# Optimization experiments

Hardware: AMD Instinct MI355X
Metric: run time of the kernel (lower is better)

Reference implementation:

```python
import jax, jax.numpy as jnp
import numpy as np

EMBED_DIM = 512
NUM_HEADS = 8
HEAD_DIM = EMBED_DIM // NUM_HEADS
BATCH = 2
SEQ = 4096
LN_EPS = 1e-5


def setup_inputs() -> dict:
    key = jax.random.key(0)
    ks = jax.random.split(key, 10)
    s = 1.0 / np.sqrt(EMBED_DIM)
    d = dict(
        x=jax.random.normal(ks[0], (BATCH, SEQ, EMBED_DIM), dtype=jnp.float32),
        wq=jax.random.normal(ks[1], (EMBED_DIM, EMBED_DIM), dtype=jnp.float32) * s,
        bq=jnp.zeros((EMBED_DIM,), jnp.float32),
        wk=jax.random.normal(ks[2], (EMBED_DIM, EMBED_DIM), dtype=jnp.float32) * s,
        bk=jnp.zeros((EMBED_DIM,), jnp.float32),
        wv=jax.random.normal(ks[3], (EMBED_DIM, EMBED_DIM), dtype=jnp.float32) * s,
        bv=jnp.zeros((EMBED_DIM,), jnp.float32),
        wo=jax.random.normal(ks[4], (EMBED_DIM, EMBED_DIM), dtype=jnp.float32) * s,
        bo=jnp.zeros((EMBED_DIM,), jnp.float32),
        ln_g=jnp.ones((EMBED_DIM,), jnp.float32),
        ln_b=jnp.zeros((EMBED_DIM,), jnp.float32),
    )
    return d


def reference(x, wq, bq, wk, bk, wv, bv, wo, bo, ln_g, ln_b):
    B, S, E = x.shape
    H, D = NUM_HEADS, HEAD_DIM
    residual = x
    # QKV projections (weights stored [in, out])
    q = (x @ wq + bq).reshape(B, S, H, D).transpose(0, 2, 1, 3)  # [B,H,S,D]
    k = (x @ wk + bk).reshape(B, S, H, D).transpose(0, 2, 1, 3)
    v = (x @ wv + bv).reshape(B, S, H, D).transpose(0, 2, 1, 3)
    # scaled dot-product attention
    scores = jnp.einsum('bhsd,bhtd->bhst', q, k) / jnp.sqrt(jnp.float32(D))
    attn = jax.nn.softmax(scores, axis=-1)
    ctx = jnp.einsum('bhst,bhtd->bhsd', attn, v)  # [B,H,S,D]
    ctx = ctx.transpose(0, 2, 1, 3).reshape(B, S, E)
    # output projection (dropout=0 in eval) + residual + LayerNorm
    out = ctx @ wo + bo
    y = out + residual
    mu = jnp.mean(y, axis=-1, keepdims=True)
    var = jnp.var(y, axis=-1, keepdims=True)
    y = (y - mu) * jax.lax.rsqrt(var + LN_EPS) * ln_g + ln_b
    return y
```

## Files before the change

kernel.cpp:

```cpp
#include <hip/hip_runtime.h>


typedef unsigned short u16;
typedef unsigned int u32;
typedef short bf16x8 __attribute__((ext_vector_type(8)));
typedef float f32x2 __attribute__((ext_vector_type(2)));
typedef float f32x4 __attribute__((ext_vector_type(4)));
typedef float f32x8 __attribute__((ext_vector_type(8)));
typedef float f32x16 __attribute__((ext_vector_type(16)));
typedef unsigned short u16x4 __attribute__((ext_vector_type(4)));
typedef unsigned int u32x2 __attribute__((ext_vector_type(2)));
typedef unsigned int u32x4 __attribute__((ext_vector_type(4)));

#define S_LEN 4096
#define E_DIM 512
#define H_NUM 8
#define D_DIM 64
#define M_ROWS 8192

#define Q_SCALE 0.18033688011112042f

static __device__ __forceinline__ u16 f2bf(float f) {
    unsigned int u = __float_as_uint(f);
    u += 0x7fffu + ((u >> 16) & 1u);
    return (u16)(u >> 16);
}

static __device__ __forceinline__ u32 cvt_pk_bf16(float a, float b) {
    u32 r;
    asm("v_cvt_pk_bf16_f32 %0, %1, %2" : "=v"(r) : "v"(a), "v"(b));
    return r;
}

#if __has_builtin(__builtin_amdgcn_exp2f)
#define EXP2(x) __builtin_amdgcn_exp2f(x)
#else
static __device__ __forceinline__ float exp2_hw(float x) {
    float r;
    asm volatile("v_exp_f32 %0, %1\n\ts_nop 1" : "=v"(r) : "v"(x));
    return r;
}
#define EXP2(x) exp2_hw(x)
#endif

static __device__ __forceinline__ float vsum16(f32x16 v) {
    f32x8 a = __builtin_shufflevector(v, v, 0, 1, 2, 3, 4, 5, 6, 7) +
              __builtin_shufflevector(v, v, 8, 9, 10, 11, 12, 13, 14, 15);
    f32x4 b = __builtin_shufflevector(a, a, 0, 1, 2, 3) +
              __builtin_shufflevector(a, a, 4, 5, 6, 7);
    f32x2 c = __builtin_shufflevector(b, b, 0, 1) +
              __builtin_shufflevector(b, b, 2, 3);
    return c[0] + c[1];
}

static __device__ __forceinline__ void gload_lds16(const u16* g, u16* l) {
    __builtin_amdgcn_global_load_lds(
        (const __attribute__((address_space(1))) u32*)g,
        (__attribute__((address_space(3))) u32*)l, 16, 0, 0);
}

__global__ __launch_bounds__(256) void cvt_k(const float* __restrict__ src,
                                             u16* __restrict__ dst, int n4) {
    int i = blockIdx.x * 256 + threadIdx.x;
    if (i >= n4) return;
    float4 v = ((const float4*)src)[i];
    u16x4 o;
    o[0] = f2bf(v.x); o[1] = f2bf(v.y); o[2] = f2bf(v.z); o[3] = f2bf(v.w);
    ((u16x4*)dst)[i] = o;
}

__global__ __launch_bounds__(256) void cvtT4_k(
    const float* __restrict__ w0, const float* __restrict__ w1,
    const float* __restrict__ w2, const float* __restrict__ w3,
    u16* __restrict__ o0, u16* __restrict__ o1,
    u16* __restrict__ o2, u16* __restrict__ o3)
{
    __shared__ float fT[64][68];
    const int g = blockIdx.x;
    const int which = g >> 6;
    const int tile = g & 63;
    const int k0 = (tile >> 3) * 64, n0 = (tile & 7) * 64;
    const float* w = which == 0 ? w0 : which == 1 ? w1 : which == 2 ? w2 : w3;
    u16* o = which == 0 ? o0 : which == 1 ? o1 : which == 2 ? o2 : o3;
    const int tr = threadIdx.x >> 4, tc = threadIdx.x & 15;
    #pragma unroll
    for (int p = 0; p < 4; p++) {
        const int kr = p * 16 + tr;
        float4 v = *(const float4*)&w[(size_t)(k0 + kr) * 512 + n0 + tc * 4];
        fT[tc * 4 + 0][kr] = v.x;
        fT[tc * 4 + 1][kr] = v.y;
        fT[tc * 4 + 2][kr] = v.z;
        fT[tc * 4 + 3][kr] = v.w;
    }
    __syncthreads();
    #pragma unroll
    for (int p = 0; p < 4; p++) {
        const int nr = p * 16 + tr;
        u16x4 ov;
        ov[0] = f2bf(fT[nr][tc * 4 + 0]);
        ov[1] = f2bf(fT[nr][tc * 4 + 1]);
        ov[2] = f2bf(fT[nr][tc * 4 + 2]);
        ov[3] = f2bf(fT[nr][tc * 4 + 3]);
        *(u16x4*)&o[(size_t)(n0 + nr) * 512 + k0 + tc * 4] = ov;
    }
}

template <int BM, int BN, int MODE>
__global__ __launch_bounds__(256) void gemm_k(
    const u16* __restrict__ A,
    const u16* __restrict__ Wt0, const u16* __restrict__ Wt1,
    const u16* __restrict__ Wt2,
    const float* __restrict__ b0, const float* __restrict__ b1,
    const float* __restrict__ b2,
    u16* __restrict__ q_out, u16* __restrict__ k_out, u16* __restrict__ vt_out,
    const float* __restrict__ resid, float* __restrict__ of32)
{
    constexpr int FM = BM / 32, FN = BN / 32;
    __shared__ __align__(16) u16 Asm[BM * 32];
    __shared__ __align__(16) u16 Bsm[BN * 32];

    const int t = threadIdx.x, wave = t >> 6, lane = t & 63;
    constexpr int nb_per = 512 / BN;
    int sel, bn;
    if (MODE == 0) { sel = blockIdx.x / nb_per; bn = blockIdx.x % nb_per; }
    else           { sel = 0;                   bn = blockIdx.x; }
    const int bm = blockIdx.y;

    const u16* Wt = (MODE == 0) ? (sel == 0 ? Wt0 : (sel == 1 ? Wt1 : Wt2)) : Wt0;
    const float* bias = (MODE == 0) ? (sel == 0 ? b0 : (sel == 1 ? b1 : b2)) : b0;

    const int wm = (wave >> 1) * (BM / 2);
    const int wn = (wave & 1) * (BN / 2);
    const int lrow = lane & 15, kq = (lane >> 4) * 8;

    f32x4 acc[FM][FN];
    #pragma unroll
    for (int i = 0; i < FM; i++)
        #pragma unroll
        for (int j = 0; j < FN; j++)
            acc[i][j] = (f32x4){0.f, 0.f, 0.f, 0.f};

    const u16* Ag = A + (size_t)bm * BM * 512 + (size_t)(t >> 2) * 512 + (t & 3) * 8;
    const u16* Bg = Wt + (size_t)bn * BN * 512 + (size_t)(t >> 2) * 512 + (t & 3) * 8;
    u16* Al = Asm + (size_t)wave * 512;
    u16* Bl = Bsm + (size_t)wave * 512;

    for (int kk = 0; kk < 512; kk += 32) {
        #pragma unroll
        for (int p = 0; p < BM / 32; p++)
            gload_lds16(Ag + (size_t)p * 64 * 512 + kk, Al + p * 2048);
        #pragma unroll
        for (int p = 0; p < BN / 32; p++)
            gload_lds16(Bg + (size_t)p * 64 * 512 + kk, Bl + p * 2048);
        __syncthreads();

        bf16x8 af[FM], bfv[FN];
        #pragma unroll
        for (int i = 0; i < FM; i++)
            af[i] = *(const bf16x8*)&Asm[(wm + i * 16 + lrow) * 32 + kq];
        #pragma unroll
        for (int j = 0; j < FN; j++)
            bfv[j] = *(const bf16x8*)&Bsm[(wn + j * 16 + lrow) * 32 + kq];
        #pragma unroll
        for (int i = 0; i < FM; i++)
            #pragma unroll
            for (int j = 0; j < FN; j++)
                acc[i][j] = __builtin_amdgcn_mfma_f32_16x16x32_bf16(
                    af[i], bfv[j], acc[i][j], 0, 0, 0);
        __syncthreads();
    }

    #pragma unroll
    for (int i = 0; i < FM; i++) {
        #pragma unroll
        for (int j = 0; j < FN; j++) {
            const int col = bn * BN + wn + j * 16 + lrow;
            const float bcol = bias[col];
            const int row0 = bm * BM + wm + i * 16 + (lane >> 4) * 4;
            if (MODE == 0) {
                const int b = row0 >> 12, s0v = row0 & 4095;
                const int h = col >> 6,  d = col & 63;
                if (sel == 2) {
                    u16x4 pk;
                    #pragma unroll
                    for (int q = 0; q < 4; q++)
                        pk[q] = f2bf(acc[i][j][q] + bcol);
                    *(u16x4*)&vt_out[(((size_t)(b * 8 + h)) * 64 + d) * 4096 + s0v] = pk;
                } else {
                    u16* o = (sel == 0) ? q_out : k_out;
                    const float sc = (sel == 0) ? Q_SCALE : 1.0f;
                    #pragma unroll
                    for (int q = 0; q < 4; q++)
                        o[(((size_t)(b * 8 + h)) * 4096 + s0v + q) * 64 + d] =
                            f2bf((acc[i][j][q] + bcol) * sc);
                }
            } else {
                #pragma unroll
                for (int q = 0; q < 4; q++) {
                    const size_t idx = (size_t)(row0 + q) * 512 + col;
                    of32[idx] = acc[i][j][q] + bcol + resid[idx];
                }
            }
        }
    }
}

__global__ __launch_bounds__(512, 2) void attn_k(
    const u16* __restrict__ Q, const u16* __restrict__ K,
    const u16* __restrict__ Vt, u16* __restrict__ ctx)
{
    __shared__ __align__(16) u16 SM[32768];

    const int t = threadIdx.x, w = t >> 6, lane = t & 63;
    const int l31 = lane & 31, hi = lane >> 5;
    const int kh = w >> 2, wl = w & 3;

    const int bid = blockIdx.x;
    const int xcd = bid & 7, j = bid >> 3;
    const int head = xcd * 2 + (j & 1);
    const int qt = j >> 1;

    const u16* Qb = Q + (size_t)head * S_LEN * D_DIM;
    const u16* Kb = K + (size_t)head * S_LEN * D_DIM;
    const u16* Vb = Vt + (size_t)head * D_DIM * S_LEN;
    const int q0w = qt * 256 + wl * 64;

    bf16x8 qfA[4], qfB[4];
    #pragma unroll
    for (int ks = 0; ks < 4; ks++) {
        qfA[ks] = *(const bf16x8*)&Qb[(size_t)(q0w + l31) * 64 + ks * 16 + hi * 8];
        qfB[ks] = *(const bf16x8*)&Qb[(size_t)(q0w + 32 + l31) * 64 + ks * 16 + hi * 8];
    }

    u16* const KH = SM + kh * 16384;
    u16* const VH = KH + 8192;

    const u16* kp[8];
    const u16* vp[8];
    #pragma unroll
    for (int i = 0; i < 8; i++) {
        const int r = (i >> 2) * 32 + l31;
        const int c = (i & 3) * 2 + hi;
        const int phys = r * 8 + (c ^ (r & 7));
        kp[i] = KH + phys * 8;
        vp[i] = VH + phys * 8;
    }

    f32x16 acc0A = {0.f}, acc1A = {0.f}, acc0B = {0.f}, acc1B = {0.f};
    float lA = 0.f, lB = 0.f;

    const int th = t & 255;
    const int c0 = th, c1 = th + 256;
    const int sr0 = c0 >> 3, sc0 = (c0 & 7) ^ (sr0 & 7);
    const int sr1 = c1 >> 3, sc1 = (c1 & 7) ^ (sr1 & 7);
    const u16* kg0 = Kb + (size_t)(kh * 2048 + sr0) * 64 + sc0 * 8;
    const u16* kg1 = Kb + (size_t)(kh * 2048 + sr1) * 64 + sc1 * 8;
    const u16* vg0 = Vb + (size_t)sr0 * S_LEN + kh * 2048 + sc0 * 8;
    const u16* vg1 = Vb + (size_t)sr1 * S_LEN + kh * 2048 + sc1 * 8;
    u16* const kd0 = KH + wl * 512;
    u16* const kd1 = KH + 2048 + wl * 512;
    u16* const vd0 = VH + wl * 512;
    u16* const vd1 = VH + 2048 + wl * 512;

#define ATTN_STAGE(DST)                                                      \
    {                                                                        \
        gload_lds16(kg0, kd0 + (DST)); gload_lds16(kg1, kd1 + (DST));        \
        gload_lds16(vg0, vd0 + (DST)); gload_lds16(vg1, vd1 + (DST));        \
        kg0 += 4096; kg1 += 4096; vg0 += 64; vg1 += 64;                      \
    }

#define ATTN_COMPUTE(BUF)                                                    \
    {                                                                        \
        f32x16 sA0 = {0.f}, sA1 = {0.f}, sB0 = {0.f}, sB1 = {0.f};           \
        __builtin_amdgcn_s_setprio(1);                                       \
        _Pragma("unroll")                                                    \
        for (int ks = 0; ks < 4; ks++) {                                     \
            bf16x8 ka = *(const bf16x8*)(kp[ks] + (BUF));                    \
            bf16x8 kb2 = *(const bf16x8*)(kp[4 + ks] + (BUF));               \
            sA0 = __builtin_amdgcn_mfma_f32_32x32x16_bf16(ka, qfA[ks], sA0, 0, 0, 0); \
            sB0 = __builtin_amdgcn_mfma_f32_32x32x16_bf16(ka, qfB[ks], sB0, 0, 0, 0); \
            sA1 = __builtin_amdgcn_mfma_f32_32x32x16_bf16(kb2, qfA[ks], sA1, 0, 0, 0); \
            sB1 = __builtin_amdgcn_mfma_f32_32x32x16_bf16(kb2, qfB[ks], sB1, 0, 0, 0); \
        }                                                                    \
        __builtin_amdgcn_s_setprio(0);                                       \
        _Pragma("unroll")                                                    \
        for (int e = 0; e < 16; e++) {                                       \
            sA0[e] = EXP2(sA0[e]); sA1[e] = EXP2(sA1[e]);                    \
            sB0[e] = EXP2(sB0[e]); sB1[e] = EXP2(sB1[e]);                    \
        }                                                                    \
        lA += vsum16(sA0 + sA1);                                             \
        lB += vsum16(sB0 + sB1);                                             \
        bf16x8 pfA[4], pfB[4];                                               \
        _Pragma("unroll")                                                    \
        for (int ks = 0; ks < 4; ks++) {                                     \
            const int r0 = (ks & 1) * 8;                                     \
            const f32x16& sa = (ks < 2) ? sA0 : sA1;                         \
            u32 ax1 = cvt_pk_bf16(sa[r0 + 0], sa[r0 + 1]);                   \
            u32 ay1 = cvt_pk_bf16(sa[r0 + 4], sa[r0 + 5]);                   \
            asm("v_permlane32_swap_b32 %0, %1" : "+v"(ax1), "+v"(ay1));      \
            u32 ax2 = cvt_pk_bf16(sa[r0 + 2], sa[r0 + 3]);                   \
            u32 ay2 = cvt_pk_bf16(sa[r0 + 6], sa[r0 + 7]);                   \
            asm("v_permlane32_swap_b32 %0, %1" : "+v"(ax2), "+v"(ay2));      \
            u32x4 wva; wva[0] = ax1; wva[1] = ax2; wva[2] = ay1; wva[3] = ay2; \
            pfA[ks] = *(bf16x8*)&wva;                                        \
            const f32x16& sb = (ks < 2) ? sB0 : sB1;                         \
            u32 bx1 = cvt_pk_bf16(sb[r0 + 0], sb[r0 + 1]);                   \
            u32 by1 = cvt_pk_bf16(sb[r0 + 4], sb[r0 + 5]);                   \
            asm("v_permlane32_swap_b32 %0, %1" : "+v"(bx1), "+v"(by1));      \
            u32 bx2 = cvt_pk_bf16(sb[r0 + 2], sb[r0 + 3]);                   \
            u32 by2 = cvt_pk_bf16(sb[r0 + 6], sb[r0 + 7]);                   \
            asm("v_permlane32_swap_b32 %0, %1" : "+v"(bx2), "+v"(by2));      \
            u32x4 wvb; wvb[0] = bx1; wvb[1] = bx2; wvb[2] = by1; wvb[3] = by2; \
            pfB[ks] = *(bf16x8*)&wvb;                                        \
        }                                                                    \
        __builtin_amdgcn_s_setprio(1);                                       \
        _Pragma("unroll")                                                    \
        for (int ks = 0; ks < 4; ks++) {                                     \
            bf16x8 va = *(const bf16x8*)(vp[ks] + (BUF));                    \
            bf16x8 vb2 = *(const bf16x8*)(vp[4 + ks] + (BUF));               \
            acc0A = __builtin_amdgcn_mfma_f32_32x32x16_bf16(va, pfA[ks], acc0A, 0, 0, 0); \
            acc0B = __builtin_amdgcn_mfma_f32_32x32x16_bf16(va, pfB[ks], acc0B, 0, 0, 0); \
            acc1A = __builtin_amdgcn_mfma_f32_32x32x16_bf16(vb2, pfA[ks], acc1A, 0, 0, 0); \
            acc1B = __builtin_amdgcn_mfma_f32_32x32x16_bf16(vb2, pfB[ks], acc1B, 0, 0, 0); \
        }                                                                    \
        __builtin_amdgcn_s_setprio(0);                                       \
    }

    ATTN_STAGE(0);
    __syncthreads();

    for (int it = 0; it < 16; ++it) {
        ATTN_STAGE(4096);
        ATTN_COMPUTE(0);
        __syncthreads();
        if (it != 15) ATTN_STAGE(0);
        ATTN_COMPUTE(4096);
        __syncthreads();
    }

    __syncthreads();
    float* const cb = (float*)SM;
    float* const p = cb + (size_t)(wl * 64 + lane) * 34;
    if (kh == 1) {
        #pragma unroll
        for (int e = 0; e < 16; e++) { p[e] = acc0A[e]; p[16 + e] = acc0B[e]; }
        p[32] = lA; p[33] = lB;
    }
    __syncthreads();
    if (kh == 0) {
        #pragma unroll
        for (int e = 0; e < 16; e++) { acc0A[e] += p[e]; acc0B[e] += p[16 + e]; }
        lA += p[32]; lB += p[33];
    }
    __syncthreads();
    if (kh == 1) {
        #pragma unroll
        for (int e = 0; e < 16; e++) { p[e] = acc1A[e]; p[16 + e] = acc1B[e]; }
    }
    __syncthreads();
    if (kh == 0) {
        #pragma unroll
        for (int e = 0; e < 16; e++) { acc1A[e] += p[e]; acc1B[e] += p[16 + e]; }
        lA += __shfl_xor(lA, 32);
        lB += __shfl_xor(lB, 32);

        const int b = head >> 3, h = head & 7;
        const float liA = 1.0f / lA, liB = 1.0f / lB;
        const size_t oA = (size_t)(b * S_LEN + q0w + l31) * 512 + h * 64 + 4 * hi;
        const size_t oB = oA + (size_t)32 * 512;
        #pragma unroll
        for (int rq = 0; rq < 4; rq++) {
            u32x2 wa;
            wa[0] = cvt_pk_bf16(acc0A[4 * rq + 0] * liA, acc0A[4 * rq + 1] * liA);
            wa[1] = cvt_pk_bf16(acc0A[4 * rq + 2] * liA, acc0A[4 * rq + 3] * liA);
            *(u32x2*)&ctx[oA + 8 * rq] = wa;
            wa[0] = cvt_pk_bf16(acc1A[4 * rq + 0] * liA, acc1A[4 * rq + 1] * liA);
            wa[1] = cvt_pk_bf16(acc1A[4 * rq + 2] * liA, acc1A[4 * rq + 3] * liA);
            *(u32x2*)&ctx[oA + 32 + 8 * rq] = wa;
            wa[0] = cvt_pk_bf16(acc0B[4 * rq + 0] * liB, acc0B[4 * rq + 1] * liB);
            wa[1] = cvt_pk_bf16(acc0B[4 * rq + 2] * liB, acc0B[4 * rq + 3] * liB);
            *(u32x2*)&ctx[oB + 8 * rq] = wa;
            wa[0] = cvt_pk_bf16(acc1B[4 * rq + 0] * liB, acc1B[4 * rq + 1] * liB);
            wa[1] = cvt_pk_bf16(acc1B[4 * rq + 2] * liB, acc1B[4 * rq + 3] * liB);
            *(u32x2*)&ctx[oB + 32 + 8 * rq] = wa;
        }
    }
#undef ATTN_STAGE
#undef ATTN_COMPUTE
}

__global__ __launch_bounds__(256) void ln_k(const float* __restrict__ y,
                                            const float* __restrict__ g,
                                            const float* __restrict__ beta,
                                            float* __restrict__ out)
{
    const int w = threadIdx.x >> 6, lane = threadIdx.x & 63;
    const size_t row = (size_t)blockIdx.x * 4 + w;
    const float4* yr = (const float4*)(y + row * 512);
    float4 a = yr[lane], b = yr[lane + 64];
    float s  = a.x + a.y + a.z + a.w + b.x + b.y + b.z + b.w;
    float ss = a.x*a.x + a.y*a.y + a.z*a.z + a.w*a.w
             + b.x*b.x + b.y*b.y + b.z*b.z + b.w*b.w;
    #pragma unroll
    for (int o = 1; o < 64; o <<= 1) {
        s  += __shfl_xor(s, o);
        ss += __shfl_xor(ss, o);
    }
    const float mu  = s * (1.0f / 512.0f);
    const float var = ss * (1.0f / 512.0f) - mu * mu;
    const float inv = rsqrtf(var + 1e-5f);
    const float4* g4 = (const float4*)g;
    const float4* b4 = (const float4*)beta;
    float4 ga = g4[lane], gb = g4[lane + 64];
    float4 ba = b4[lane], bb = b4[lane + 64];
    float4 oa, ob;
    oa.x = (a.x - mu) * inv * ga.x + ba.x;
    oa.y = (a.y - mu) * inv * ga.y + ba.y;
    oa.z = (a.z - mu) * inv * ga.z + ba.z;
    oa.w = (a.w - mu) * inv * ga.w + ba.w;
    ob.x = (b.x - mu) * inv * gb.x + bb.x;
    ob.y = (b.y - mu) * inv * gb.y + bb.y;
    ob.z = (b.z - mu) * inv * gb.z + bb.z;
    ob.w = (b.w - mu) * inv * gb.w + bb.w;
    float4* orow = (float4*)(out + row * 512);
    orow[lane] = oa;
    orow[lane + 64] = ob;
}

extern "C" void kernel_launch(void* const* d_in, const int* in_sizes, int n_in,
                              void* d_out, int out_size, void* d_ws, size_t ws_size,
                              hipStream_t stream)
{
    const float* x    = (const float*)d_in[0];
    const float* wq   = (const float*)d_in[1];
    const float* bq   = (const float*)d_in[2];
    const float* wk   = (const float*)d_in[3];
    const float* bk   = (const float*)d_in[4];
    const float* wv   = (const float*)d_in[5];
    const float* bv   = (const float*)d_in[6];
    const float* wo   = (const float*)d_in[7];
    const float* bo   = (const float*)d_in[8];
    const float* ln_g = (const float*)d_in[9];
    const float* ln_b = (const float*)d_in[10];

    char* ws = (char*)d_ws;
    u16* xb   = (u16*)(ws);
    u16* wqt  = (u16*)(ws + 8388608);
    u16* wkt  = (u16*)(ws + 8912896);
    u16* wvt  = (u16*)(ws + 9437184);
    u16* wot  = (u16*)(ws + 9961472);
    u16* Qb   = (u16*)(ws + 10485760);
    u16* Kb   = (u16*)(ws + 18874368);
    u16* Vtb  = (u16*)(ws + 27262976);
    u16* ctxb = (u16*)(ws + 35651584);
    float* yb = (float*)(ws + 10485760);

    cvt_k<<<4096, 256, 0, stream>>>(x, xb, (M_ROWS * E_DIM) / 4);
    cvtT4_k<<<256, 256, 0, stream>>>(wq, wk, wv, wo, wqt, wkt, wvt, wot);

    gemm_k<128, 128, 0><<<dim3(12, 64), 256, 0, stream>>>(
        xb, wqt, wkt, wvt, bq, bk, bv, Qb, Kb, Vtb, nullptr, nullptr);

    attn_k<<<256, 512, 0, stream>>>(Qb, Kb, Vtb, ctxb);

    gemm_k<128, 64, 2><<<dim3(8, 64), 256, 0, stream>>>(
        ctxb, wot, wot, wot, bo, bo, bo, nullptr, nullptr, nullptr, x, yb);

    ln_k<<<2048, 256, 0, stream>>>(yb, ln_g, ln_b, (float*)d_out);
}
```

Measured before the change: 150.9 us.

## Split attention KV range across four wave groups with 1024-thread blocks

The attention kernel now launches 1024 threads per block, giving four groups of four waves. Each group processes a quarter of the key/value sequence, using 32-key tiles per stage instead of 64, and the LDS layout and swizzle are reworked to match. Partial outputs and row sums are then reduced through shared memory in four combine rounds. The aim is more waves per block to hide latency, at the cost of smaller MFMA batches per stage, more barriers in the reduction, and a lower per-thread register budget.

```diff
diff --git a/kernel.cpp b/kernel.cpp
--- a/kernel.cpp
+++ b/kernel.cpp
@@ -205,7 +205,7 @@
     }
 }
 
-__global__ __launch_bounds__(512, 2) void attn_k(
+__global__ __launch_bounds__(1024) void attn_k(
     const u16* __restrict__ Q, const u16* __restrict__ K,
     const u16* __restrict__ Vt, u16* __restrict__ ctx)
 {
@@ -232,96 +232,87 @@
         qfB[ks] = *(const bf16x8*)&Qb[(size_t)(q0w + 32 + l31) * 64 + ks * 16 + hi * 8];
     }
 
-    u16* const KH = SM + kh * 16384;
-    u16* const VH = KH + 8192;
-
-    const u16* kp[8];
-    const u16* vp[8];
-    #pragma unroll
-    for (int i = 0; i < 8; i++) {
-        const int r = (i >> 2) * 32 + l31;
-        const int c = (i & 3) * 2 + hi;
-        const int phys = r * 8 + (c ^ (r & 7));
-        kp[i] = KH + phys * 8;
-        vp[i] = VH + phys * 8;
+    u16* const KQ = SM + kh * 8192;
+
+    const u16* kp[4];
+    const u16* vp[4];
+    #pragma unroll
+    for (int ks = 0; ks < 4; ks++) {
+        const int c = ks * 2 + hi;
+        kp[ks] = KQ + (l31 * 8 + (c ^ (l31 & 7))) * 8;
+    }
+    #pragma unroll
+    for (int i = 0; i < 4; i++) {
+        const int dblk = i >> 1, ks2 = i & 1;
+        const int r = dblk * 32 + l31;
+        const int c = ks2 * 2 + hi;
+        vp[i] = KQ + 4096 + (r * 4 + (c ^ ((r >> 1) & 3))) * 8;
     }
 
     f32x16 acc0A = {0.f}, acc1A = {0.f}, acc0B = {0.f}, acc1B = {0.f};
     float lA = 0.f, lB = 0.f;
 
     const int th = t & 255;
-    const int c0 = th, c1 = th + 256;
-    const int sr0 = c0 >> 3, sc0 = (c0 & 7) ^ (sr0 & 7);
-    const int sr1 = c1 >> 3, sc1 = (c1 & 7) ^ (sr1 & 7);
-    const u16* kg0 = Kb + (size_t)(kh * 2048 + sr0) * 64 + sc0 * 8;
-    const u16* kg1 = Kb + (size_t)(kh * 2048 + sr1) * 64 + sc1 * 8;
-    const u16* vg0 = Vb + (size_t)sr0 * S_LEN + kh * 2048 + sc0 * 8;
-    const u16* vg1 = Vb + (size_t)sr1 * S_LEN + kh * 2048 + sc1 * 8;
-    u16* const kd0 = KH + wl * 512;
-    u16* const kd1 = KH + 2048 + wl * 512;
-    u16* const vd0 = VH + wl * 512;
-    u16* const vd1 = VH + 2048 + wl * 512;
+    const int kr = th >> 3, kc = (th & 7) ^ (kr & 7);
+    const int vr = th >> 2, vc = (th & 3) ^ ((vr >> 1) & 3);
+    const u16* kg = Kb + (size_t)(kh * 1024 + kr) * 64 + kc * 8;
+    const u16* vg = Vb + (size_t)vr * S_LEN + kh * 1024 + vc * 8;
+    u16* const kd = KQ + wl * 512;
+    u16* const vd = KQ + 4096 + wl * 512;
 
 #define ATTN_STAGE(DST)                                                      \
     {                                                                        \
-        gload_lds16(kg0, kd0 + (DST)); gload_lds16(kg1, kd1 + (DST));        \
-        gload_lds16(vg0, vd0 + (DST)); gload_lds16(vg1, vd1 + (DST));        \
-        kg0 += 4096; kg1 += 4096; vg0 += 64; vg1 += 64;                      \
+        gload_lds16(kg, kd + (DST)); gload_lds16(vg, vd + (DST));            \
+        kg += 2048; vg += 32;                                                \
     }
 
 #define ATTN_COMPUTE(BUF)                                                    \
     {                                                                        \
-        f32x16 sA0 = {0.f}, sA1 = {0.f}, sB0 = {0.f}, sB1 = {0.f};           \
+        f32x16 sA = {0.f}, sB = {0.f};                                       \
         __builtin_amdgcn_s_setprio(1);                                       \
         _Pragma("unroll")                                                    \
         for (int ks = 0; ks < 4; ks++) {                                     \
             bf16x8 ka = *(const bf16x8*)(kp[ks] + (BUF));                    \
-            bf16x8 kb2 = *(const bf16x8*)(kp[4 + ks] + (BUF));               \
-            sA0 = __builtin_amdgcn_mfma_f32_32x32x16_bf16(ka, qfA[ks], sA0, 0, 0, 0); \
-            sB0 = __builtin_amdgcn_mfma_f32_32x32x16_bf16(ka, qfB[ks], sB0, 0, 0, 0); \
-            sA1 = __builtin_amdgcn_mfma_f32_32x32x16_bf16(kb2, qfA[ks], sA1, 0, 0, 0); \
-            sB1 = __builtin_amdgcn_mfma_f32_32x32x16_bf16(kb2, qfB[ks], sB1, 0, 0, 0); \
+            sA = __builtin_amdgcn_mfma_f32_32x32x16_bf16(ka, qfA[ks], sA, 0, 0, 0); \
+            sB = __builtin_amdgcn_mfma_f32_32x32x16_bf16(ka, qfB[ks], sB, 0, 0, 0); \
         }                                                                    \
         __builtin_amdgcn_s_setprio(0);                                       \
         _Pragma("unroll")                                                    \
         for (int e = 0; e < 16; e++) {                                       \
-            sA0[e] = EXP2(sA0[e]); sA1[e] = EXP2(sA1[e]);                    \
-            sB0[e] = EXP2(sB0[e]); sB1[e] = EXP2(sB1[e]);                    \
+            sA[e] = EXP2(sA[e]); sB[e] = EXP2(sB[e]);                        \
         }                                                                    \
-        lA += vsum16(sA0 + sA1);                                             \
-        lB += vsum16(sB0 + sB1);                                             \
-        bf16x8 pfA[4], pfB[4];                                               \
-        _Pragma("unroll")                                                    \
-        for (int ks = 0; ks < 4; ks++) {                                     \
-            const int r0 = (ks & 1) * 8;                                     \
-            const f32x16& sa = (ks < 2) ? sA0 : sA1;                         \
-            u32 ax1 = cvt_pk_bf16(sa[r0 + 0], sa[r0 + 1]);                   \
-            u32 ay1 = cvt_pk_bf16(sa[r0 + 4], sa[r0 + 5]);                   \
+        lA += vsum16(sA);                                                    \
+        lB += vsum16(sB);                                                    \
+        bf16x8 pfA[2], pfB[2];                                               \
+        _Pragma("unroll")                                                    \
+        for (int ks2 = 0; ks2 < 2; ks2++) {                                  \
+            const int r0 = ks2 * 8;                                          \
+            u32 ax1 = cvt_pk_bf16(sA[r0 + 0], sA[r0 + 1]);                   \
+            u32 ay1 = cvt_pk_bf16(sA[r0 + 4], sA[r0 + 5]);                   \
             asm("v_permlane32_swap_b32 %0, %1" : "+v"(ax1), "+v"(ay1));      \
-            u32 ax2 = cvt_pk_bf16(sa[r0 + 2], sa[r0 + 3]);                   \
-            u32 ay2 = cvt_pk_bf16(sa[r0 + 6], sa[r0 + 7]);                   \
+            u32 ax2 = cvt_pk_bf16(sA[r0 + 2], sA[r0 + 3]);                   \
+            u32 ay2 = cvt_pk_bf16(sA[r0 + 6], sA[r0 + 7]);                   \
             asm("v_permlane32_swap_b32 %0, %1" : "+v"(ax2), "+v"(ay2));      \
             u32x4 wva; wva[0] = ax1; wva[1] = ax2; wva[2] = ay1; wva[3] = ay2; \
-            pfA[ks] = *(bf16x8*)&wva;                                        \
-            const f32x16& sb = (ks < 2) ? sB0 : sB1;                         \
-            u32 bx1 = cvt_pk_bf16(sb[r0 + 0], sb[r0 + 1]);                   \
-            u32 by1 = cvt_pk_bf16(sb[r0 + 4], sb[r0 + 5]);                   \
+            pfA[ks2] = *(bf16x8*)&wva;                                       \
+            u32 bx1 = cvt_pk_bf16(sB[r0 + 0], sB[r0 + 1]);                   \
+            u32 by1 = cvt_pk_bf16(sB[r0 + 4], sB[r0 + 5]);                   \
             asm("v_permlane32_swap_b32 %0, %1" : "+v"(bx1), "+v"(by1));      \
-            u32 bx2 = cvt_pk_bf16(sb[r0 + 2], sb[r0 + 3]);                   \
-            u32 by2 = cvt_pk_bf16(sb[r0 + 6], sb[r0 + 7]);                   \
+            u32 bx2 = cvt_pk_bf16(sB[r0 + 2], sB[r0 + 3]);                   \
+            u32 by2 = cvt_pk_bf16(sB[r0 + 6], sB[r0 + 7]);                   \
             asm("v_permlane32_swap_b32 %0, %1" : "+v"(bx2), "+v"(by2));      \
             u32x4 wvb; wvb[0] = bx1; wvb[1] = bx2; wvb[2] = by1; wvb[3] = by2; \
-            pfB[ks] = *(bf16x8*)&wvb;                                        \
+            pfB[ks2] = *(bf16x8*)&wvb;                                       \
         }                                                                    \
         __builtin_amdgcn_s_setprio(1);                                       \
         _Pragma("unroll")                                                    \
-        for (int ks = 0; ks < 4; ks++) {                                     \
-            bf16x8 va = *(const bf16x8*)(vp[ks] + (BUF));                    \
-            bf16x8 vb2 = *(const bf16x8*)(vp[4 + ks] + (BUF));               \
-            acc0A = __builtin_amdgcn_mfma_f32_32x32x16_bf16(va, pfA[ks], acc0A, 0, 0, 0); \
-            acc0B = __builtin_amdgcn_mfma_f32_32x32x16_bf16(va, pfB[ks], acc0B, 0, 0, 0); \
-            acc1A = __builtin_amdgcn_mfma_f32_32x32x16_bf16(vb2, pfA[ks], acc1A, 0, 0, 0); \
-            acc1B = __builtin_amdgcn_mfma_f32_32x32x16_bf16(vb2, pfB[ks], acc1B, 0, 0, 0); \
+        for (int ks2 = 0; ks2 < 2; ks2++) {                                  \
+            bf16x8 v0 = *(const bf16x8*)(vp[ks2] + (BUF));                   \
+            bf16x8 v1 = *(const bf16x8*)(vp[2 + ks2] + (BUF));               \
+            acc0A = __builtin_amdgcn_mfma_f32_32x32x16_bf16(v0, pfA[ks2], acc0A, 0, 0, 0); \
+            acc0B = __builtin_amdgcn_mfma_f32_32x32x16_bf16(v0, pfB[ks2], acc0B, 0, 0, 0); \
+            acc1A = __builtin_amdgcn_mfma_f32_32x32x16_bf16(v1, pfA[ks2], acc1A, 0, 0, 0); \
+            acc1B = __builtin_amdgcn_mfma_f32_32x32x16_bf16(v1, pfB[ks2], acc1B, 0, 0, 0); \
         }                                                                    \
         __builtin_amdgcn_s_setprio(0);                                       \
     }
@@ -330,37 +321,40 @@
     __syncthreads();
 
     for (int it = 0; it < 16; ++it) {
-        ATTN_STAGE(4096);
+        ATTN_STAGE(2048);
         ATTN_COMPUTE(0);
         __syncthreads();
         if (it != 15) ATTN_STAGE(0);
-        ATTN_COMPUTE(4096);
+        ATTN_COMPUTE(2048);
         __syncthreads();
     }
 
-    __syncthreads();
     float* const cb = (float*)SM;
-    float* const p = cb + (size_t)(wl * 64 + lane) * 34;
-    if (kh == 1) {
-        #pragma unroll
-        for (int e = 0; e < 16; e++) { p[e] = acc0A[e]; p[16 + e] = acc0B[e]; }
-        p[32] = lA; p[33] = lB;
-    }
-    __syncthreads();
+#define COMBINE(ACC, EXTRA_W, EXTRA_R)                                       \
+    __syncthreads();                                                         \
+    if (kh) {                                                                \
+        float* p = cb + (size_t)(((kh - 1) * 4 + wl) * 64 + lane) * 17;      \
+        _Pragma("unroll")                                                    \
+        for (int e = 0; e < 16; e++) p[e] = ACC[e];                          \
+        EXTRA_W;                                                             \
+    }                                                                        \
+    __syncthreads();                                                         \
+    if (!kh) {                                                               \
+        _Pragma("unroll")                                                    \
+        for (int jj = 0; jj < 3; jj++) {                                     \
+            const float* p = cb + (size_t)((jj * 4 + wl) * 64 + lane) * 17;  \
+            _Pragma("unroll")                                                \
+            for (int e = 0; e < 16; e++) ACC[e] += p[e];                     \
+            EXTRA_R;                                                         \
+        }                                                                    \
+    }
+    COMBINE(acc0A, p[16] = lA, lA += p[16])
+    COMBINE(acc0B, p[16] = lB, lB += p[16])
+    COMBINE(acc1A, , )
+    COMBINE(acc1B, , )
+#undef COMBINE
+
     if (kh == 0) {
-        #pragma unroll
-        for (int e = 0; e < 16; e++) { acc0A[e] += p[e]; acc0B[e] += p[16 + e]; }
-        lA += p[32]; lB += p[33];
-    }
-    __syncthreads();
-    if (kh == 1) {
-        #pragma unroll
-        for (int e = 0; e < 16; e++) { p[e] = acc1A[e]; p[16 + e] = acc1B[e]; }
-    }
-    __syncthreads();
-    if (kh == 0) {
-        #pragma unroll
-        for (int e = 0; e < 16; e++) { acc1A[e] += p[e]; acc1B[e] += p[16 + e]; }
         lA += __shfl_xor(lA, 32);
         lB += __shfl_xor(lB, 32);
 
@@ -461,7 +455,7 @@
     gemm_k<128, 128, 0><<<dim3(12, 64), 256, 0, stream>>>(
         xb, wqt, wkt, wvt, bq, bk, bv, Qb, Kb, Vtb, nullptr, nullptr);
 
-    attn_k<<<256, 512, 0, stream>>>(Qb, Kb, Vtb, ctxb);
+    attn_k<<<256, 1024, 0, stream>>>(Qb, Kb, Vtb, ctxb);
 
     gemm_k<128, 64, 2><<<dim3(8, 64), 256, 0, stream>>>(
         ctxb, wot, wot, wot, bo, bo, bo, nullptr, nullptr, nullptr, x, yb);
```

Measured after the change: 267.2 us. 1.77x slower.

## Split attention over two key halves and merge partials in a combine kernel

Applied to the files above, without the earlier changes.

The attention grid doubles from 256 to 512 blocks, and each block now processes only half of the key sequence, so the loop runs 8 iterations instead of 16. Each half writes an unnormalized bf16 context and its per-row softmax denominators into reused workspace buffers. A new combine kernel adds the two partials and divides by the summed denominators. This is meant to fill all CUs at two blocks each. The cost is an extra launch, extra global traffic, and bf16 rounding of the unnormalized partial sums.

```diff
diff --git a/kernel.cpp b/kernel.cpp
--- a/kernel.cpp
+++ b/kernel.cpp
@@ -24,6 +24,9 @@
     unsigned int u = __float_as_uint(f);
     u += 0x7fffu + ((u >> 16) & 1u);
     return (u16)(u >> 16);
+}
+static __device__ __forceinline__ float bf2f(u16 h) {
+    return __uint_as_float(((unsigned int)h) << 16);
 }
 
 static __device__ __forceinline__ u32 cvt_pk_bf16(float a, float b) {
@@ -207,7 +210,9 @@
 
 __global__ __launch_bounds__(512, 2) void attn_k(
     const u16* __restrict__ Q, const u16* __restrict__ K,
-    const u16* __restrict__ Vt, u16* __restrict__ ctx)
+    const u16* __restrict__ Vt, u16* __restrict__ pctx0,
+    u16* __restrict__ pctx1, float* __restrict__ pl0,
+    float* __restrict__ pl1)
 {
     __shared__ __align__(16) u16 SM[32768];
 
@@ -218,12 +223,15 @@
     const int bid = blockIdx.x;
     const int xcd = bid & 7, j = bid >> 3;
     const int head = xcd * 2 + (j & 1);
-    const int qt = j >> 1;
+    const int jj2 = j >> 1;
+    const int qt = jj2 & 15;
+    const int keyH = jj2 >> 4;
 
     const u16* Qb = Q + (size_t)head * S_LEN * D_DIM;
     const u16* Kb = K + (size_t)head * S_LEN * D_DIM;
     const u16* Vb = Vt + (size_t)head * D_DIM * S_LEN;
     const int q0w = qt * 256 + wl * 64;
+    const int key0 = keyH * 2048 + kh * 1024;
 
     bf16x8 qfA[4], qfB[4];
     #pragma unroll
@@ -253,10 +261,10 @@
     const int c0 = th, c1 = th + 256;
     const int sr0 = c0 >> 3, sc0 = (c0 & 7) ^ (sr0 & 7);
     const int sr1 = c1 >> 3, sc1 = (c1 & 7) ^ (sr1 & 7);
-    const u16* kg0 = Kb + (size_t)(kh * 2048 + sr0) * 64 + sc0 * 8;
-    const u16* kg1 = Kb + (size_t)(kh * 2048 + sr1) * 64 + sc1 * 8;
-    const u16* vg0 = Vb + (size_t)sr0 * S_LEN + kh * 2048 + sc0 * 8;
-    const u16* vg1 = Vb + (size_t)sr1 * S_LEN + kh * 2048 + sc1 * 8;
+    const u16* kg0 = Kb + (size_t)(key0 + sr0) * 64 + sc0 * 8;
+    const u16* kg1 = Kb + (size_t)(key0 + sr1) * 64 + sc1 * 8;
+    const u16* vg0 = Vb + (size_t)sr0 * S_LEN + key0 + sc0 * 8;
+    const u16* vg1 = Vb + (size_t)sr1 * S_LEN + key0 + sc1 * 8;
     u16* const kd0 = KH + wl * 512;
     u16* const kd1 = KH + 2048 + wl * 512;
     u16* const vd0 = VH + wl * 512;
@@ -329,11 +337,11 @@
     ATTN_STAGE(0);
     __syncthreads();
 
-    for (int it = 0; it < 16; ++it) {
+    for (int it = 0; it < 8; ++it) {
         ATTN_STAGE(4096);
         ATTN_COMPUTE(0);
         __syncthreads();
-        if (it != 15) ATTN_STAGE(0);
+        if (it != 7) ATTN_STAGE(0);
         ATTN_COMPUTE(4096);
         __syncthreads();
     }
@@ -364,29 +372,53 @@
         lA += __shfl_xor(lA, 32);
         lB += __shfl_xor(lB, 32);
 
+        u16* const pc = keyH ? pctx1 : pctx0;
+        float* const pl = keyH ? pl1 : pl0;
         const int b = head >> 3, h = head & 7;
-        const float liA = 1.0f / lA, liB = 1.0f / lB;
+        if (hi == 0) {
+            pl[head * 4096 + q0w + l31] = lA;
+            pl[head * 4096 + q0w + 32 + l31] = lB;
+        }
         const size_t oA = (size_t)(b * S_LEN + q0w + l31) * 512 + h * 64 + 4 * hi;
         const size_t oB = oA + (size_t)32 * 512;
         #pragma unroll
         for (int rq = 0; rq < 4; rq++) {
             u32x2 wa;
-            wa[0] = cvt_pk_bf16(acc0A[4 * rq + 0] * liA, acc0A[4 * rq + 1] * liA);
-            wa[1] = cvt_pk_bf16(acc0A[4 * rq + 2] * liA, acc0A[4 * rq + 3] * liA);
-            *(u32x2*)&ctx[oA + 8 * rq] = wa;
-            wa[0] = cvt_pk_bf16(acc1A[4 * rq + 0] * liA, acc1A[4 * rq + 1] * liA);
-            wa[1] = cvt_pk_bf16(acc1A[4 * rq + 2] * liA, acc1A[4 * rq + 3] * liA);
-            *(u32x2*)&ctx[oA + 32 + 8 * rq] = wa;
-            wa[0] = cvt_pk_bf16(acc0B[4 * rq + 0] * liB, acc0B[4 * rq + 1] * liB);
-            wa[1] = cvt_pk_bf16(acc0B[4 * rq + 2] * liB, acc0B[4 * rq + 3] * liB);
-            *(u32x2*)&ctx[oB + 8 * rq] = wa;
-            wa[0] = cvt_pk_bf16(acc1B[4 * rq + 0] * liB, acc1B[4 * rq + 1] * liB);
-            wa[1] = cvt_pk_bf16(acc1B[4 * rq + 2] * liB, acc1B[4 * rq + 3] * liB);
-            *(u32x2*)&ctx[oB + 32 + 8 * rq] = wa;
+            wa[0] = cvt_pk_bf16(acc0A[4 * rq + 0], acc0A[4 * rq + 1]);
+            wa[1] = cvt_pk_bf16(acc0A[4 * rq + 2], acc0A[4 * rq + 3]);
+            *(u32x2*)&pc[oA + 8 * rq] = wa;
+            wa[0] = cvt_pk_bf16(acc1A[4 * rq + 0], acc1A[4 * rq + 1]);
+            wa[1] = cvt_pk_bf16(acc1A[4 * rq + 2], acc1A[4 * rq + 3]);
+            *(u32x2*)&pc[oA + 32 + 8 * rq] = wa;
+            wa[0] = cvt_pk_bf16(acc0B[4 * rq + 0], acc0B[4 * rq + 1]);
+            wa[1] = cvt_pk_bf16(acc0B[4 * rq + 2], acc0B[4 * rq + 3]);
+            *(u32x2*)&pc[oB + 8 * rq] = wa;
+            wa[0] = cvt_pk_bf16(acc1B[4 * rq + 0], acc1B[4 * rq + 1]);
+            wa[1] = cvt_pk_bf16(acc1B[4 * rq + 2], acc1B[4 * rq + 3]);
+            *(u32x2*)&pc[oB + 32 + 8 * rq] = wa;
         }
     }
 #undef ATTN_STAGE
 #undef ATTN_COMPUTE
+}
+
+__global__ __launch_bounds__(256) void comb_k(
+    const u16* __restrict__ p1, const float* __restrict__ l0,
+    const float* __restrict__ l1, u16* __restrict__ p0io)
+{
+    const int i = blockIdx.x * 256 + threadIdx.x;
+    const int row = i >> 7, col0 = (i & 127) * 4;
+    const int b = row >> 12, s = row & 4095, h = col0 >> 6;
+    const int hd = b * 8 + h;
+    const float li = 1.0f / (l0[hd * 4096 + s] + l1[hd * 4096 + s]);
+    const size_t idx = (size_t)row * 512 + col0;
+    u16x4 a = *(const u16x4*)&p0io[idx];
+    u16x4 c = *(const u16x4*)&p1[idx];
+    u16x4 o;
+    #pragma unroll
+    for (int jv = 0; jv < 4; jv++)
+        o[jv] = f2bf((bf2f(a[jv]) + bf2f(c[jv])) * li);
+    *(u16x4*)&p0io[idx] = o;
 }
 
 __global__ __launch_bounds__(256) void ln_k(const float* __restrict__ y,
@@ -454,6 +486,8 @@
     u16* Vtb  = (u16*)(ws + 27262976);
     u16* ctxb = (u16*)(ws + 35651584);
     float* yb = (float*)(ws + 10485760);
+    float* pl0 = (float*)(ws + 8388608);
+    float* pl1 = (float*)(ws + 8912896);
 
     cvt_k<<<4096, 256, 0, stream>>>(x, xb, (M_ROWS * E_DIM) / 4);
     cvtT4_k<<<256, 256, 0, stream>>>(wq, wk, wv, wo, wqt, wkt, wvt, wot);
@@ -461,7 +495,8 @@
     gemm_k<128, 128, 0><<<dim3(12, 64), 256, 0, stream>>>(
         xb, wqt, wkt, wvt, bq, bk, bv, Qb, Kb, Vtb, nullptr, nullptr);
 
-    attn_k<<<256, 512, 0, stream>>>(Qb, Kb, Vtb, ctxb);
+    attn_k<<<512, 512, 0, stream>>>(Qb, Kb, Vtb, ctxb, xb, pl0, pl1);
+    comb_k<<<4096, 256, 0, stream>>>(xb, pl0, pl1, ctxb);
 
     gemm_k<128, 64, 2><<<dim3(8, 64), 256, 0, stream>>>(
         ctxb, wot, wot, wot, bo, bo, bo, nullptr, nullptr, nullptr, x, yb);
```

New measurement: 164.7 us. +9.2%, slower.

## Software-pipeline attention QK and PV across tiles; merge conversion kernels

Applied to the files above, without the earlier changes.

Splits the attention tile computation into QK, exp/pack, and PV phases and software-pipelines them, so the QK MFMAs for the next key tile are issued while the softmax exp and PV of the previous tile proceed. K and V staging are decoupled so each buffer is refilled at a different point. Separately, the x and weight conversion kernels are merged into one launch to save a kernel launch. The pipelining doubles the live score registers, which risks register pressure and lower occupancy.

```diff
diff --git a/kernel.cpp b/kernel.cpp
--- a/kernel.cpp
+++ b/kernel.cpp
@@ -59,24 +59,23 @@
         (__attribute__((address_space(3))) u32*)l, 16, 0, 0);
 }
 
-__global__ __launch_bounds__(256) void cvt_k(const float* __restrict__ src,
-                                             u16* __restrict__ dst, int n4) {
-    int i = blockIdx.x * 256 + threadIdx.x;
-    if (i >= n4) return;
-    float4 v = ((const float4*)src)[i];
-    u16x4 o;
-    o[0] = f2bf(v.x); o[1] = f2bf(v.y); o[2] = f2bf(v.z); o[3] = f2bf(v.w);
-    ((u16x4*)dst)[i] = o;
-}
-
-__global__ __launch_bounds__(256) void cvtT4_k(
+__global__ __launch_bounds__(256) void cvt_all_k(
+    const float* __restrict__ x, u16* __restrict__ xb,
     const float* __restrict__ w0, const float* __restrict__ w1,
     const float* __restrict__ w2, const float* __restrict__ w3,
     u16* __restrict__ o0, u16* __restrict__ o1,
     u16* __restrict__ o2, u16* __restrict__ o3)
 {
     __shared__ float fT[64][68];
-    const int g = blockIdx.x;
+    if (blockIdx.x < 4096) {
+        int i = blockIdx.x * 256 + threadIdx.x;
+        float4 v = ((const float4*)x)[i];
+        u16x4 o;
+        o[0] = f2bf(v.x); o[1] = f2bf(v.y); o[2] = f2bf(v.z); o[3] = f2bf(v.w);
+        ((u16x4*)xb)[i] = o;
+        return;
+    }
+    const int g = blockIdx.x - 4096;
     const int which = g >> 6;
     const int tile = g & 63;
     const int k0 = (tile >> 3) * 64, n0 = (tile & 7) * 64;
@@ -248,6 +247,9 @@
 
     f32x16 acc0A = {0.f}, acc1A = {0.f}, acc0B = {0.f}, acc1B = {0.f};
     float lA = 0.f, lB = 0.f;
+    f32x16 sE0A, sE1A, sE0B, sE1B;
+    f32x16 sO0A, sO1A, sO0B, sO1B;
+    bf16x8 pfA[4], pfB[4];
 
     const int th = t & 255;
     const int c0 = th, c1 = th + 256;
@@ -262,39 +264,43 @@
     u16* const vd0 = VH + wl * 512;
     u16* const vd1 = VH + 2048 + wl * 512;
 
-#define ATTN_STAGE(DST)                                                      \
+#define STAGE_K(DST)                                                         \
+    { gload_lds16(kg0, kd0 + (DST)); gload_lds16(kg1, kd1 + (DST));          \
+      kg0 += 4096; kg1 += 4096; }
+#define STAGE_V(DST)                                                         \
+    { gload_lds16(vg0, vd0 + (DST)); gload_lds16(vg1, vd1 + (DST));          \
+      vg0 += 64; vg1 += 64; }
+
+#define QK_PH(BUF, S0A, S1A, S0B, S1B)                                       \
     {                                                                        \
-        gload_lds16(kg0, kd0 + (DST)); gload_lds16(kg1, kd1 + (DST));        \
-        gload_lds16(vg0, vd0 + (DST)); gload_lds16(vg1, vd1 + (DST));        \
-        kg0 += 4096; kg1 += 4096; vg0 += 64; vg1 += 64;                      \
-    }
-
-#define ATTN_COMPUTE(BUF)                                                    \
-    {                                                                        \
-        f32x16 sA0 = {0.f}, sA1 = {0.f}, sB0 = {0.f}, sB1 = {0.f};           \
+        S0A = (f32x16){0.f}; S1A = (f32x16){0.f};                            \
+        S0B = (f32x16){0.f}; S1B = (f32x16){0.f};                            \
         __builtin_amdgcn_s_setprio(1);                                       \
         _Pragma("unroll")                                                    \
         for (int ks = 0; ks < 4; ks++) {                                     \
             bf16x8 ka = *(const bf16x8*)(kp[ks] + (BUF));                    \
             bf16x8 kb2 = *(const bf16x8*)(kp[4 + ks] + (BUF));               \
-            sA0 = __builtin_amdgcn_mfma_f32_32x32x16_bf16(ka, qfA[ks], sA0, 0, 0, 0); \
-            sB0 = __builtin_amdgcn_mfma_f32_32x32x16_bf16(ka, qfB[ks], sB0, 0, 0, 0); \
-            sA1 = __builtin_amdgcn_mfma_f32_32x32x16_bf16(kb2, qfA[ks], sA1, 0, 0, 0); \
-            sB1 = __builtin_amdgcn_mfma_f32_32x32x16_bf16(kb2, qfB[ks], sB1, 0, 0, 0); \
+            S0A = __builtin_amdgcn_mfma_f32_32x32x16_bf16(ka, qfA[ks], S0A, 0, 0, 0); \
+            S0B = __builtin_amdgcn_mfma_f32_32x32x16_bf16(ka, qfB[ks], S0B, 0, 0, 0); \
+            S1A = __builtin_amdgcn_mfma_f32_32x32x16_bf16(kb2, qfA[ks], S1A, 0, 0, 0); \
+            S1B = __builtin_amdgcn_mfma_f32_32x32x16_bf16(kb2, qfB[ks], S1B, 0, 0, 0); \
         }                                                                    \
         __builtin_amdgcn_s_setprio(0);                                       \
+    }
+
+#define EXPPACK(S0A, S1A, S0B, S1B)                                          \
+    {                                                                        \
         _Pragma("unroll")                                                    \
         for (int e = 0; e < 16; e++) {                                       \
-            sA0[e] = EXP2(sA0[e]); sA1[e] = EXP2(sA1[e]);                    \
-            sB0[e] = EXP2(sB0[e]); sB1[e] = EXP2(sB1[e]);                    \
+            S0A[e] = EXP2(S0A[e]); S1A[e] = EXP2(S1A[e]);                    \
+            S0B[e] = EXP2(S0B[e]); S1B[e] = EXP2(S1B[e]);                    \
         }                                                                    \
-        lA += vsum16(sA0 + sA1);                                             \
-        lB += vsum16(sB0 + sB1);                                             \
-        bf16x8 pfA[4], pfB[4];                                               \
+        lA += vsum16(S0A + S1A);                                             \
+        lB += vsum16(S0B + S1B);                                             \
         _Pragma("unroll")                                                    \
         for (int ks = 0; ks < 4; ks++) {                                     \
             const int r0 = (ks & 1) * 8;                                     \
-            const f32x16& sa = (ks < 2) ? sA0 : sA1;                         \
+            const f32x16& sa = (ks < 2) ? S0A : S1A;                         \
             u32 ax1 = cvt_pk_bf16(sa[r0 + 0], sa[r0 + 1]);                   \
             u32 ay1 = cvt_pk_bf16(sa[r0 + 4], sa[r0 + 5]);                   \
             asm("v_permlane32_swap_b32 %0, %1" : "+v"(ax1), "+v"(ay1));      \
@@ -303,7 +309,7 @@
             asm("v_permlane32_swap_b32 %0, %1" : "+v"(ax2), "+v"(ay2));      \
             u32x4 wva; wva[0] = ax1; wva[1] = ax2; wva[2] = ay1; wva[3] = ay2; \
             pfA[ks] = *(bf16x8*)&wva;                                        \
-            const f32x16& sb = (ks < 2) ? sB0 : sB1;                         \
+            const f32x16& sb = (ks < 2) ? S0B : S1B;                         \
             u32 bx1 = cvt_pk_bf16(sb[r0 + 0], sb[r0 + 1]);                   \
             u32 by1 = cvt_pk_bf16(sb[r0 + 4], sb[r0 + 5]);                   \
             asm("v_permlane32_swap_b32 %0, %1" : "+v"(bx1), "+v"(by1));      \
@@ -313,6 +319,10 @@
             u32x4 wvb; wvb[0] = bx1; wvb[1] = bx2; wvb[2] = by1; wvb[3] = by2; \
             pfB[ks] = *(bf16x8*)&wvb;                                        \
         }                                                                    \
+    }
+
+#define PV_PH(BUF)                                                           \
+    {                                                                        \
         __builtin_amdgcn_s_setprio(1);                                       \
         _Pragma("unroll")                                                    \
         for (int ks = 0; ks < 4; ks++) {                                     \
@@ -326,17 +336,31 @@
         __builtin_amdgcn_s_setprio(0);                                       \
     }
 
-    ATTN_STAGE(0);
-    __syncthreads();
-
-    for (int it = 0; it < 16; ++it) {
-        ATTN_STAGE(4096);
-        ATTN_COMPUTE(0);
+    STAGE_K(0); STAGE_V(0);
+    __syncthreads();
+    STAGE_K(4096);
+    QK_PH(0, sE0A, sE1A, sE0B, sE1B);
+    __syncthreads();
+
+    for (int it = 0; it < 15; ++it) {
+        STAGE_K(0); STAGE_V(4096);
+        QK_PH(4096, sO0A, sO1A, sO0B, sO1B);
+        EXPPACK(sE0A, sE1A, sE0B, sE1B);
+        PV_PH(0);
         __syncthreads();
-        if (it != 15) ATTN_STAGE(0);
-        ATTN_COMPUTE(4096);
+        STAGE_K(4096); STAGE_V(0);
+        QK_PH(0, sE0A, sE1A, sE0B, sE1B);
+        EXPPACK(sO0A, sO1A, sO0B, sO1B);
+        PV_PH(4096);
         __syncthreads();
     }
+    STAGE_V(4096);
+    QK_PH(4096, sO0A, sO1A, sO0B, sO1B);
+    EXPPACK(sE0A, sE1A, sE0B, sE1B);
+    PV_PH(0);
+    __syncthreads();
+    EXPPACK(sO0A, sO1A, sO0B, sO1B);
+    PV_PH(4096);
 
     __syncthreads();
     float* const cb = (float*)SM;
@@ -385,8 +409,11 @@
             *(u32x2*)&ctx[oB + 32 + 8 * rq] = wa;
         }
     }
-#undef ATTN_STAGE
-#undef ATTN_COMPUTE
+#undef STAGE_K
+#undef STAGE_V
+#undef QK_PH
+#undef EXPPACK
+#undef PV_PH
 }
 
 __global__ __launch_bounds__(256) void ln_k(const float* __restrict__ y,
@@ -455,8 +482,8 @@
     u16* ctxb = (u16*)(ws + 35651584);
     float* yb = (float*)(ws + 10485760);
 
-    cvt_k<<<4096, 256, 0, stream>>>(x, xb, (M_ROWS * E_DIM) / 4);
-    cvtT4_k<<<256, 256, 0, stream>>>(wq, wk, wv, wo, wqt, wkt, wvt, wot);
+    cvt_all_k<<<4352, 256, 0, stream>>>(x, xb, wq, wk, wv, wo,
+                                        wqt, wkt, wvt, wot);
 
     gemm_k<128, 128, 0><<<dim3(12, 64), 256, 0, stream>>>(
         xb, wqt, wkt, wvt, bq, bk, bv, Qb, Kb, Vtb, nullptr, nullptr);
```

After: 342.6 us. +127.1%, slower.
